# Optimization experiments

Hardware: AMD Instinct MI355X
Metric: run time of the kernel (lower is better)

Reference implementation:

```python
import jax, jax.numpy as jnp
import numpy as np

N_HEADS = 16


def setup_inputs() -> dict:
    key = jax.random.key(0)
    ks = jax.random.split(key, 9)
    B, S, D = 2, 2048, 1024
    s = 0.02
    return {
        "x": jax.random.normal(ks[0], (B, S, D), dtype=jnp.float32),
        "Wq": jax.random.normal(ks[1], (D, D), dtype=jnp.float32) * s,
        "bq": jax.random.normal(ks[2], (D,), dtype=jnp.float32) * s,
        "Wk": jax.random.normal(ks[3], (D, D), dtype=jnp.float32) * s,
        "bk": jax.random.normal(ks[4], (D,), dtype=jnp.float32) * s,
        "Wv": jax.random.normal(ks[5], (D, D), dtype=jnp.float32) * s,
        "bv": jax.random.normal(ks[6], (D,), dtype=jnp.float32) * s,
        "Wo": jax.random.normal(ks[7], (D, D), dtype=jnp.float32) * s,
        "bo": jax.random.normal(ks[8], (D,), dtype=jnp.float32) * s,
    }


def reference(x, Wq, bq, Wk, bk, Wv, bv, Wo, bo):
    B, S, D = x.shape
    H = N_HEADS
    hd = D // H
    # projections -> [B, H, S, hd]
    def heads(w, b):
        return (x @ w + b).reshape(B, S, H, hd).transpose(0, 2, 1, 3)
    Q, K, V = heads(Wq, bq), heads(Wk, bk), heads(Wv, bv)
    scores = jnp.einsum("bhqd,bhkd->bhqk", Q, K)
    causal = jnp.triu(jnp.ones((S, S), dtype=bool), k=1)  # True above diagonal
    scores = jnp.where(causal, -jnp.inf, scores)
    w = jax.nn.softmax(scores / jnp.sqrt(jnp.float32(hd)), axis=-1)
    ctx = jnp.einsum("bhqk,bhkd->bhqd", w, V).transpose(0, 2, 1, 3).reshape(B, S, D)
    return ctx @ Wo + bo
```

## Files before the change

### kernel.cpp

```cpp
#include <hip/hip_runtime.h>
#include <hip/hip_bf16.h>

typedef __attribute__((ext_vector_type(8))) short short8;
typedef __attribute__((ext_vector_type(4))) float floatx4;
typedef __attribute__((ext_vector_type(4))) int intx4;

#define D_MODEL 1024
#define SEQ     2048
#define NB      2
#define NH      16
#define HD      64
#define MROWS   4096
#define CZ      (0.125f * 1.44269504f)

__device__ __forceinline__ floatx4 mfma_bf16(short8 a, short8 b, floatx4 c) {
  return __builtin_amdgcn_mfma_f32_16x16x32_bf16(a, b, c, 0, 0, 0);
}

__device__ __forceinline__ void dma16(const __hip_bfloat16* g, __hip_bfloat16* l) {
  __builtin_amdgcn_global_load_lds(
      (const __attribute__((address_space(1))) void*)g,
      (__attribute__((address_space(3))) void*)l, 16, 0, 0);
}
#define WAIT_VM(n)  __asm__ __volatile__("s_waitcnt vmcnt(" #n ")" ::: "memory")
#define BARRIER()   __asm__ __volatile__("s_barrier" ::: "memory")
#define WAIT_LGKM() __asm__ __volatile__("s_waitcnt lgkmcnt(0)" ::: "memory")

__device__ __forceinline__ int pack2bf(float a, float b) {
  unsigned ua = __builtin_bit_cast(unsigned, a) + 0x8000u;
  unsigned ub = __builtin_bit_cast(unsigned, b) + 0x8000u;
  return (int)__builtin_amdgcn_perm(ub, ua, 0x07060302u);
}

__global__ void prep_kernel(const float* __restrict__ x, __hip_bfloat16* __restrict__ xb,
                            const float* __restrict__ W0, const float* __restrict__ W1,
                            const float* __restrict__ W2, const float* __restrict__ W3,
                            __hip_bfloat16* __restrict__ T0, __hip_bfloat16* __restrict__ T1,
                            __hip_bfloat16* __restrict__ T2, __hip_bfloat16* __restrict__ T3) {
  const int z = blockIdx.z;
  if (z == 4) {
    const int tid = threadIdx.y * 32 + threadIdx.x;
    const int base = ((blockIdx.y * 32 + blockIdx.x) * 256 + tid) * 16;
#pragma unroll
    for (int c = 0; c < 4; c++) {
      float4 v = *(const float4*)(x + base + c * 4);
      __hip_bfloat16 tmp[4];
      tmp[0] = __float2bfloat16(v.x);
      tmp[1] = __float2bfloat16(v.y);
      tmp[2] = __float2bfloat16(v.z);
      tmp[3] = __float2bfloat16(v.w);
      *(ushort4*)(xb + base + c * 4) = *(ushort4*)tmp;
    }
    return;
  }
  const float* W = (z == 0) ? W0 : (z == 1) ? W1 : (z == 2) ? W2 : W3;
  __hip_bfloat16* Wt = (z == 0) ? T0 : (z == 1) ? T1 : (z == 2) ? T2 : T3;
  __shared__ float tile[32][33];
  int k0 = blockIdx.x * 32, n0 = blockIdx.y * 32;
  int tx = threadIdx.x, ty = threadIdx.y;
#pragma unroll
  for (int i = 0; i < 4; i++)
    tile[ty + 8 * i][tx] = W[(size_t)(k0 + ty + 8 * i) * D_MODEL + n0 + tx];
  __syncthreads();
#pragma unroll
  for (int i = 0; i < 4; i++)
    Wt[(size_t)(n0 + ty + 8 * i) * D_MODEL + k0 + tx] = __float2bfloat16(tile[tx][ty + 8 * i]);
}

template <int MODE>
__global__ __launch_bounds__(256) void gemm_kernel(
    const __hip_bfloat16* __restrict__ X,
    const __hip_bfloat16* __restrict__ Wt0, const __hip_bfloat16* __restrict__ Wt1,
    const __hip_bfloat16* __restrict__ Wt2,
    const float* __restrict__ b0, const float* __restrict__ b1, const float* __restrict__ b2,
    void* __restrict__ out0, void* __restrict__ out1, void* __restrict__ out2) {
  constexpr int MT = (MODE == 0) ? 128 : 64;
  constexpr int I = MT / 32;
  constexpr int NKT = D_MODEL / 32;

  const int z = blockIdx.y;
  const __hip_bfloat16* Wt = (z == 0) ? Wt0 : (z == 1) ? Wt1 : Wt2;
  const float* bias = (z == 0) ? b0 : (z == 1) ? b1 : b2;
  void* outp = (z == 0) ? out0 : (z == 1) ? out1 : out2;
  const float scale = (MODE == 0 && z == 0) ? CZ : 1.f;

  __shared__ __attribute__((aligned(16))) __hip_bfloat16 As[3][MT * 32];
  __shared__ __attribute__((aligned(16))) __hip_bfloat16 Bs[3][128 * 32];

  const int n0 = blockIdx.x * 128;
  const int m0 = blockIdx.z * MT;
  const int t = threadIdx.x;
  const int lane = t & 63, w = t >> 6;
  const int wm = (w >> 1) * (MT / 2), wn = (w & 1) * 64;
  const int lr = lane & 15;
  const int lq = lane >> 4;

  const __hip_bfloat16* Xp = X + (size_t)m0 * D_MODEL;
  const __hip_bfloat16* Wp = Wt + (size_t)n0 * D_MODEL;

  const int lrow = lane >> 2;
  const int skg = (lane & 3) << 3;
  const int srowA = ((MT == 128) ? (w << 5) : (w << 4)) + lrow;
  const int sbA0 = (((MT == 128) ? (w << 5) : (w << 4)) << 5);
  const int sbA1 = sbA0 + (16 << 5);
  const int srowB = (w << 5) + lrow;
  const int sbB0 = ((w << 5) << 5);
  const int sbB1 = sbB0 + (16 << 5);

#define STAGE_G(kt_, buf_)                                                              \
  {                                                                                     \
    const int kn_ = (kt_) * 32;                                                         \
    dma16(Xp + (size_t)srowA * D_MODEL + kn_ + skg, &As[buf_][sbA0]);                   \
    if (MT == 128) dma16(Xp + (size_t)(srowA + 16) * D_MODEL + kn_ + skg, &As[buf_][sbA1]); \
    dma16(Wp + (size_t)srowB * D_MODEL + kn_ + skg, &Bs[buf_][sbB0]);                   \
    dma16(Wp + (size_t)(srowB + 16) * D_MODEL + kn_ + skg, &Bs[buf_][sbB1]);            \
  }

  floatx4 acc[I][4];
#pragma unroll
  for (int i = 0; i < I; i++)
#pragma unroll
    for (int j = 0; j < 4; j++) acc[i][j] = (floatx4){0.f, 0.f, 0.f, 0.f};

  STAGE_G(0, 0);
  STAGE_G(1, 1);

  int cb = 0;
  for (int kt = 0; kt < NKT; kt++) {
    if (kt < NKT - 1) {
      if constexpr (MODE == 0) WAIT_VM(4);
      else                     WAIT_VM(3);
    } else {
      WAIT_VM(0);
    }
    BARRIER();
    if (kt + 2 < NKT) {
      const int nb = (cb == 0) ? 2 : cb - 1;
      STAGE_G(kt + 2, nb);
    }
    const __hip_bfloat16* Ac = As[cb];
    const __hip_bfloat16* Bc = Bs[cb];
    short8 af[I], bfr[4];
#pragma unroll
    for (int i = 0; i < I; i++) af[i] = *(const short8*)&Ac[(wm + i * 16 + lr) * 32 + lq * 8];
#pragma unroll
    for (int j = 0; j < 4; j++) bfr[j] = *(const short8*)&Bc[(wn + j * 16 + lr) * 32 + lq * 8];
#pragma unroll
    for (int i = 0; i < I; i++)
#pragma unroll
      for (int j = 0; j < 4; j++) acc[i][j] = mfma_bf16(af[i], bfr[j], acc[i][j]);
    cb = (cb == 2) ? 0 : cb + 1;
  }
#undef STAGE_G

#pragma unroll
  for (int j = 0; j < 4; j++) {
    const int n = n0 + wn + j * 16 + lr;
    const float bv = bias[n];
#pragma unroll
    for (int i = 0; i < I; i++) {
      const int mb = m0 + wm + i * 16 + lq * 4;
      if (MODE == 0) {
        __hip_bfloat16* O = (__hip_bfloat16*)outp;
        const int b = mb >> 11, s = mb & 2047;
        const int h = n >> 6, d = n & 63;
        if (z == 2) {
          ushort4 pk;
          __hip_bfloat16* pp = (__hip_bfloat16*)&pk;
#pragma unroll
          for (int r = 0; r < 4; r++) pp[r] = __float2bfloat16(acc[i][j][r] + bv);
          *(ushort4*)(O + (((size_t)(b * NH + h) * HD + d) * SEQ + s)) = pk;
        } else {
#pragma unroll
          for (int r = 0; r < 4; r++)
            O[(((size_t)(b * NH + h) * SEQ + (s + r)) * HD) + d] =
                __float2bfloat16((acc[i][j][r] + bv) * scale);
        }
      } else {
#pragma unroll
        for (int r = 0; r < 4; r++)
          ((float*)outp)[(size_t)(mb + r) * D_MODEL + n] = acc[i][j][r] + bv;
      }
    }
  }
}

__global__ __launch_bounds__(256, 2) void attn_kernel(
    const __hip_bfloat16* __restrict__ Q, const __hip_bfloat16* __restrict__ Kg,
    const __hip_bfloat16* __restrict__ Vt, __hip_bfloat16* __restrict__ ctx) {
  const int bh = blockIdx.x;
  const int b = bh >> 4, h = bh & 15;
  const int p = blockIdx.y;
  const int t = threadIdx.x, lane = t & 63, w = t >> 6;
  const int lr = lane & 15, lq = lane >> 4;
  const int wr = w & 1, wb = w >> 1;

  __shared__ __attribute__((aligned(16))) __hip_bfloat16 Ks[2][128 * 64];
  __shared__ __attribute__((aligned(16))) __hip_bfloat16 VTs[2][64 * 128];
  __shared__ __attribute__((aligned(16))) float dumpO[2048];
  __shared__ float dumpL[256];

  const __hip_bfloat16* Qb = Q + (size_t)bh * SEQ * HD;
  const __hip_bfloat16* Kb = Kg + (size_t)bh * SEQ * HD;
  const __hip_bfloat16* Vb = Vt + (size_t)bh * HD * SEQ;

  short8 qf[2][2][2];
#pragma unroll
  for (int ph = 0; ph < 2; ph++) {
    const int qt = ph ? 31 - p : p;
#pragma unroll
    for (int rt = 0; rt < 2; rt++)
#pragma unroll
      for (int ks = 0; ks < 2; ks++)
        qf[ph][rt][ks] = *(const short8*)(Qb + (size_t)(qt * 64 + wr * 32 + rt * 16 + lr) * HD +
                                          ks * 32 + lq * 8);
  }

  const int krow = (w << 5) + (lane >> 3);
  const int ksl = lane & 7;
  const int vrow = (w << 4) + (lane >> 4);
  const int vsl = lane & 15;

#define STAGE(tb, nb)                                                                     \
  {                                                                                       \
    _Pragma("unroll") for (int i = 0; i < 4; i++) {                                       \
      const int r_ = krow + i * 8;                                                        \
      dma16(Kb + ((size_t)((tb) + r_) << 6) + ((ksl ^ (r_ & 7)) << 3),                    \
            &Ks[nb][((w << 5) + i * 8) << 6]);                                            \
    }                                                                                     \
    _Pragma("unroll") for (int i = 0; i < 4; i++) {                                       \
      const int r_ = vrow + i * 4;                                                        \
      dma16(Vb + (size_t)r_ * SEQ + (tb) + ((vsl ^ (r_ & 15)) << 3),                      \
            &VTs[nb][((w << 4) + i * 4) << 7]);                                           \
    }                                                                                     \
  }

  const int nktA = (p + 2) >> 1;
  const int TOT = 17;
#define KTN(gs) (((gs) < nktA) ? (gs) : (gs)-nktA)

  STAGE(0, 0);
  int g = 0;

  const int idx0 = (lr + ((lq & 1) << 5)) << 2;
  const int idx1 = idx0 + 64;
  const bool hi = (lq >= 2);

  const int kfb0 = (lr << 6) + ((lq ^ (lr & 7)) << 3);
  const int kfb1 = (lr << 6) + (((4 + lq) ^ (lr & 7)) << 3);
  const int vfb0 = (lr << 7) + ((((wb << 3) + lq) ^ lr) << 3);
  const int vfb1 = (lr << 7) + ((((wb << 3) + 4 + lq) ^ lr) << 3);
  const int kwoff = wb << 12;

  for (int ph = 0; ph < 2; ph++) {
    const int qt = ph ? 31 - p : p;
    const int nkt = (qt + 2) >> 1;
    const int qbase = qt * 64 + wr * 32;
    const int qmaxw = qbase + 31;

    floatx4 o[2][4];
#pragma unroll
    for (int rt = 0; rt < 2; rt++)
#pragma unroll
      for (int dt = 0; dt < 4; dt++) o[rt][dt] = (floatx4){0.f, 0.f, 0.f, 0.f};
    float ls[2] = {0.f, 0.f};

    for (int kt = 0; kt < nkt; kt++, g++) {
      WAIT_VM(0);
      BARRIER();
      if (g + 1 < TOT) STAGE(KTN(g + 1) << 7, (g + 1) & 1);

      const int n0w = (kt << 7) + (wb << 6);
      if (n0w <= qmaxw) {
        const int cbuf = g & 1;
        const __hip_bfloat16* Kc = &Ks[cbuf][kwoff];
        const __hip_bfloat16* Vc = VTs[cbuf];

        short8 kf[2][4];
#pragma unroll
        for (int nt = 0; nt < 4; nt++) {
          kf[0][nt] = *(const short8*)&Kc[(nt << 10) + kfb0];
          kf[1][nt] = *(const short8*)&Kc[(nt << 10) + kfb1];
        }
        floatx4 s[2][4];
#pragma unroll
        for (int rt = 0; rt < 2; rt++)
#pragma unroll
          for (int nt = 0; nt < 4; nt++) s[rt][nt] = (floatx4){0.f, 0.f, 0.f, 0.f};
#pragma unroll
        for (int ks = 0; ks < 2; ks++)
#pragma unroll
          for (int nt = 0; nt < 4; nt++) {
            s[0][nt] = mfma_bf16(kf[ks][nt], qf[ph][0][ks], s[0][nt]);
            s[1][nt] = mfma_bf16(kf[ks][nt], qf[ph][1][ks], s[1][nt]);
          }

        int pkA[2][4], pkB[2][4];
        const bool need_mask = (n0w + 63 > qbase);
#pragma unroll
        for (int rt = 0; rt < 2; rt++) {
          const int q = qbase + rt * 16 + lr;
#pragma unroll
          for (int nt = 0; nt < 4; nt++) {
            const int kbase = n0w + (nt << 4) + (lq << 2);
            float x0 = s[rt][nt][0], x1 = s[rt][nt][1], x2 = s[rt][nt][2], x3 = s[rt][nt][3];
            if (need_mask) {
              x0 = (kbase + 0 <= q) ? x0 : -1e30f;
              x1 = (kbase + 1 <= q) ? x1 : -1e30f;
              x2 = (kbase + 2 <= q) ? x2 : -1e30f;
              x3 = (kbase + 3 <= q) ? x3 : -1e30f;
            }
            const float p0 = __builtin_amdgcn_exp2f(x0);
            const float p1 = __builtin_amdgcn_exp2f(x1);
            const float p2 = __builtin_amdgcn_exp2f(x2);
            const float p3 = __builtin_amdgcn_exp2f(x3);
            ls[rt] += (p0 + p1) + (p2 + p3);
            pkA[rt][nt] = pack2bf(p0, p1);
            pkB[rt][nt] = pack2bf(p2, p3);
          }
        }

#pragma unroll
        for (int ks = 0; ks < 2; ks++) {
          short8 pf[2];
#pragma unroll
          for (int rt = 0; rt < 2; rt++) {
            const int t0 = 2 * ks, t1 = 2 * ks + 1;
            int c0a = __builtin_amdgcn_ds_bpermute(idx0, pkA[rt][t0]);
            int c0b = __builtin_amdgcn_ds_bpermute(idx0, pkA[rt][t1]);
            int c1a = __builtin_amdgcn_ds_bpermute(idx0, pkB[rt][t0]);
            int c1b = __builtin_amdgcn_ds_bpermute(idx0, pkB[rt][t1]);
            int c2a = __builtin_amdgcn_ds_bpermute(idx1, pkA[rt][t0]);
            int c2b = __builtin_amdgcn_ds_bpermute(idx1, pkA[rt][t1]);
            int c3a = __builtin_amdgcn_ds_bpermute(idx1, pkB[rt][t0]);
            int c3b = __builtin_amdgcn_ds_bpermute(idx1, pkB[rt][t1]);
            intx4 bi;
            bi[0] = hi ? c0b : c0a;
            bi[1] = hi ? c1b : c1a;
            bi[2] = hi ? c2b : c2a;
            bi[3] = hi ? c3b : c3a;
            pf[rt] = __builtin_bit_cast(short8, bi);
          }
          const int vfb = ks ? vfb1 : vfb0;
#pragma unroll
          for (int dt = 0; dt < 4; dt++) {
            short8 vf = *(const short8*)&Vc[(dt << 11) + vfb];
            o[0][dt] = mfma_bf16(vf, pf[0], o[0][dt]);
            o[1][dt] = mfma_bf16(vf, pf[1], o[1][dt]);
          }
        }
      }
    }

    const int dbase = (wr << 10) + (lane << 4);
    BARRIER();
    if (wb == 1) {
#pragma unroll
      for (int dt = 0; dt < 4; dt++) *(floatx4*)&dumpO[dbase + (dt << 2)] = o[0][dt];
      dumpL[(wr << 7) + (lane << 1)] = ls[0];
      dumpL[(wr << 7) + (lane << 1) + 1] = ls[1];
      WAIT_LGKM();
    }
    BARRIER();
    if (wb == 0) {
#pragma unroll
      for (int dt = 0; dt < 4; dt++) o[0][dt] += *(const floatx4*)&dumpO[dbase + (dt << 2)];
      ls[0] += dumpL[(wr << 7) + (lane << 1)];
      ls[1] += dumpL[(wr << 7) + (lane << 1) + 1];
    }
    BARRIER();
    if (wb == 1) {
#pragma unroll
      for (int dt = 0; dt < 4; dt++) *(floatx4*)&dumpO[dbase + (dt << 2)] = o[1][dt];
      WAIT_LGKM();
    }
    BARRIER();
    if (wb == 0) {
#pragma unroll
      for (int dt = 0; dt < 4; dt++) o[1][dt] += *(const floatx4*)&dumpO[dbase + (dt << 2)];
      float inv[2];
#pragma unroll
      for (int rt = 0; rt < 2; rt++) {
        float v = ls[rt];
        v += __shfl_xor(v, 16);
        v += __shfl_xor(v, 32);
        inv[rt] = 1.f / v;
      }
#pragma unroll
      for (int rt = 0; rt < 2; rt++) {
        const int row = qbase + rt * 16 + lr;
        __hip_bfloat16* cp = ctx + (size_t)b * SEQ * D_MODEL + (size_t)row * D_MODEL + h * HD;
#pragma unroll
        for (int dt = 0; dt < 4; dt++) {
          ushort4 pk;
          __hip_bfloat16* pp = (__hip_bfloat16*)&pk;
#pragma unroll
          for (int r = 0; r < 4; r++) pp[r] = __float2bfloat16(o[rt][dt][r] * inv[rt]);
          *(ushort4*)(cp + (dt << 4) + (lq << 2)) = pk;
        }
      }
    }
  }
#undef STAGE
#undef KTN
}

extern "C" void kernel_launch(void* const* d_in, const int* in_sizes, int n_in,
                              void* d_out, int out_size, void* d_ws, size_t ws_size,
                              hipStream_t stream) {
  const float* x  = (const float*)d_in[0];
  const float* Wq = (const float*)d_in[1];
  const float* bq = (const float*)d_in[2];
  const float* Wk = (const float*)d_in[3];
  const float* bk = (const float*)d_in[4];
  const float* Wv = (const float*)d_in[5];
  const float* bv = (const float*)d_in[6];
  const float* Wo = (const float*)d_in[7];
  const float* bo = (const float*)d_in[8];

  char* ws = (char*)d_ws;
  const size_t MB = 1u << 20;
  __hip_bfloat16* xb  = (__hip_bfloat16*)(ws + 0 * MB);
  __hip_bfloat16* wtq = (__hip_bfloat16*)(ws + 8 * MB);
  __hip_bfloat16* wtk = (__hip_bfloat16*)(ws + 10 * MB);
  __hip_bfloat16* wtv = (__hip_bfloat16*)(ws + 12 * MB);
  __hip_bfloat16* wto = (__hip_bfloat16*)(ws + 14 * MB);
  __hip_bfloat16* qb  = (__hip_bfloat16*)(ws + 16 * MB);
  __hip_bfloat16* kb  = (__hip_bfloat16*)(ws + 24 * MB);
  __hip_bfloat16* vt  = (__hip_bfloat16*)(ws + 32 * MB);
  __hip_bfloat16* ctx = xb;

  prep_kernel<<<dim3(32, 32, 5), dim3(32, 8), 0, stream>>>(x, xb, Wq, Wk, Wv, Wo,
                                                           wtq, wtk, wtv, wto);
  gemm_kernel<0><<<dim3(8, 3, 32), 256, 0, stream>>>(xb, wtq, wtk, wtv, bq, bk, bv,
                                                     (void*)qb, (void*)kb, (void*)vt);
  attn_kernel<<<dim3(32, 16), 256, 0, stream>>>(qb, kb, vt, ctx);
  gemm_kernel<1><<<dim3(8, 1, 64), 256, 0, stream>>>(ctx, wto, wto, wto, bo, bo, bo,
                                                     d_out, d_out, d_out);
}
```

Before: 194.6 us.

## Split attention into one block per query tile with 64-key tiles

Each attention block now handles one 64-row query tile instead of a pair of balanced tiles, and the grid doubles to 32x32, ordered heaviest-first. K/V tiles shrink from 128 to 64 keys, which halves shared memory so the reduction scratch can reuse the K/V buffers, and launch bounds rise to allow 4 blocks per CU. The aim is higher occupancy and more blocks to hide latency. The cost is more barriers per key, shorter per-iteration work, and reliance on heaviest-first scheduling for load balance.

```diff
diff --git a/kernel.cpp b/kernel.cpp
--- a/kernel.cpp
+++ b/kernel.cpp
@@ -185,224 +185,196 @@
   }
 }
 
-__global__ __launch_bounds__(256, 2) void attn_kernel(
+__global__ __launch_bounds__(256, 4) void attn_kernel(
     const __hip_bfloat16* __restrict__ Q, const __hip_bfloat16* __restrict__ Kg,
     const __hip_bfloat16* __restrict__ Vt, __hip_bfloat16* __restrict__ ctx) {
   const int bh = blockIdx.x;
   const int b = bh >> 4, h = bh & 15;
-  const int p = blockIdx.y;
+  const int qt = 31 - blockIdx.y;
   const int t = threadIdx.x, lane = t & 63, w = t >> 6;
   const int lr = lane & 15, lq = lane >> 4;
   const int wr = w & 1, wb = w >> 1;
 
-  __shared__ __attribute__((aligned(16))) __hip_bfloat16 Ks[2][128 * 64];
-  __shared__ __attribute__((aligned(16))) __hip_bfloat16 VTs[2][64 * 128];
-  __shared__ __attribute__((aligned(16))) float dumpO[2048];
-  __shared__ float dumpL[256];
+  __shared__ __attribute__((aligned(16))) __hip_bfloat16 Ks[2][64 * 64];
+  __shared__ __attribute__((aligned(16))) __hip_bfloat16 VTs[2][64 * 64];
 
   const __hip_bfloat16* Qb = Q + (size_t)bh * SEQ * HD;
   const __hip_bfloat16* Kb = Kg + (size_t)bh * SEQ * HD;
   const __hip_bfloat16* Vb = Vt + (size_t)bh * HD * SEQ;
 
-  short8 qf[2][2][2];
-#pragma unroll
-  for (int ph = 0; ph < 2; ph++) {
-    const int qt = ph ? 31 - p : p;
-#pragma unroll
-    for (int rt = 0; rt < 2; rt++)
-#pragma unroll
-      for (int ks = 0; ks < 2; ks++)
-        qf[ph][rt][ks] = *(const short8*)(Qb + (size_t)(qt * 64 + wr * 32 + rt * 16 + lr) * HD +
-                                          ks * 32 + lq * 8);
-  }
-
-  const int krow = (w << 5) + (lane >> 3);
-  const int ksl = lane & 7;
-  const int vrow = (w << 4) + (lane >> 4);
-  const int vsl = lane & 15;
-
-#define STAGE(tb, nb)                                                                     \
-  {                                                                                       \
-    _Pragma("unroll") for (int i = 0; i < 4; i++) {                                       \
-      const int r_ = krow + i * 8;                                                        \
-      dma16(Kb + ((size_t)((tb) + r_) << 6) + ((ksl ^ (r_ & 7)) << 3),                    \
-            &Ks[nb][((w << 5) + i * 8) << 6]);                                            \
-    }                                                                                     \
-    _Pragma("unroll") for (int i = 0; i < 4; i++) {                                       \
-      const int r_ = vrow + i * 4;                                                        \
-      dma16(Vb + (size_t)r_ * SEQ + (tb) + ((vsl ^ (r_ & 15)) << 3),                      \
-            &VTs[nb][((w << 4) + i * 4) << 7]);                                           \
-    }                                                                                     \
-  }
-
-  const int nktA = (p + 2) >> 1;
-  const int TOT = 17;
-#define KTN(gs) (((gs) < nktA) ? (gs) : (gs)-nktA)
-
+  const int qrow0 = qt * 64 + wr * 32;
+
+  short8 qf[2][2];
+#pragma unroll
+  for (int rt = 0; rt < 2; rt++)
+#pragma unroll
+    for (int ks = 0; ks < 2; ks++)
+      qf[rt][ks] = *(const short8*)(Qb + (size_t)(qrow0 + rt * 16 + lr) * HD + ks * 32 + lq * 8);
+
+  const int srow = (w << 4) + (lane >> 3);
+  const int sgl = lane & 7;
+  const int sb0 = (w << 4) << 6;
+  const int sb1 = ((w << 4) + 8) << 6;
+
+#define STAGE(tb, nb)                                                                  \
+  {                                                                                    \
+    const int r0 = srow, r1 = srow + 8;                                                \
+    dma16(Kb + ((size_t)((tb) + r0) << 6) + ((sgl ^ (r0 & 7)) << 3), &Ks[nb][sb0]);    \
+    dma16(Kb + ((size_t)((tb) + r1) << 6) + ((sgl ^ (r1 & 7)) << 3), &Ks[nb][sb1]);    \
+    dma16(Vb + (size_t)r0 * SEQ + (tb) + ((sgl ^ (r0 & 7)) << 3), &VTs[nb][sb0]);      \
+    dma16(Vb + (size_t)r1 * SEQ + (tb) + ((sgl ^ (r1 & 7)) << 3), &VTs[nb][sb1]);      \
+  }
+
+  const int nkt = qt + 1;
   STAGE(0, 0);
-  int g = 0;
+
+  floatx4 o[2][4];
+#pragma unroll
+  for (int rt = 0; rt < 2; rt++)
+#pragma unroll
+    for (int dt = 0; dt < 4; dt++) o[rt][dt] = (floatx4){0.f, 0.f, 0.f, 0.f};
+  float ls[2] = {0.f, 0.f};
 
   const int idx0 = (lr + ((lq & 1) << 5)) << 2;
   const int idx1 = idx0 + 64;
   const bool hi = (lq >= 2);
 
-  const int kfb0 = (lr << 6) + ((lq ^ (lr & 7)) << 3);
-  const int kfb1 = (lr << 6) + (((4 + lq) ^ (lr & 7)) << 3);
-  const int vfb0 = (lr << 7) + ((((wb << 3) + lq) ^ lr) << 3);
-  const int vfb1 = (lr << 7) + ((((wb << 3) + 4 + lq) ^ lr) << 3);
-  const int kwoff = wb << 12;
-
-  for (int ph = 0; ph < 2; ph++) {
-    const int qt = ph ? 31 - p : p;
-    const int nkt = (qt + 2) >> 1;
-    const int qbase = qt * 64 + wr * 32;
-    const int qmaxw = qbase + 31;
-
-    floatx4 o[2][4];
-#pragma unroll
-    for (int rt = 0; rt < 2; rt++)
-#pragma unroll
-      for (int dt = 0; dt < 4; dt++) o[rt][dt] = (floatx4){0.f, 0.f, 0.f, 0.f};
-    float ls[2] = {0.f, 0.f};
-
-    for (int kt = 0; kt < nkt; kt++, g++) {
-      WAIT_VM(0);
-      BARRIER();
-      if (g + 1 < TOT) STAGE(KTN(g + 1) << 7, (g + 1) & 1);
-
-      const int n0w = (kt << 7) + (wb << 6);
-      if (n0w <= qmaxw) {
-        const int cbuf = g & 1;
-        const __hip_bfloat16* Kc = &Ks[cbuf][kwoff];
-        const __hip_bfloat16* Vc = VTs[cbuf];
-
-        short8 kf[2][4];
-#pragma unroll
-        for (int nt = 0; nt < 4; nt++) {
-          kf[0][nt] = *(const short8*)&Kc[(nt << 10) + kfb0];
-          kf[1][nt] = *(const short8*)&Kc[(nt << 10) + kfb1];
+  const int kfb0 = ((wb << 4) + lr) << 6;
+  const int kg0 = ((lq ^ (lr & 7)) << 3);
+  const int kg1 = (((4 + lq) ^ (lr & 7)) << 3);
+  const int vg = ((((lq & 2) << 1) + (wb << 1) + (lq & 1)) ^ (lr & 7)) << 3;
+
+  for (int kt = 0; kt < nkt; kt++) {
+    WAIT_VM(0);
+    BARRIER();
+    if (kt + 1 < nkt) STAGE((kt + 1) << 6, (kt + 1) & 1);
+
+    const int kw0 = (kt << 6) + (wb << 4);
+    if (kw0 <= qrow0 + 31) {
+      const __hip_bfloat16* Kc = Ks[kt & 1];
+      const __hip_bfloat16* Vc = VTs[kt & 1];
+
+      short8 kf[2][2];
+#pragma unroll
+      for (int nt = 0; nt < 2; nt++) {
+        kf[0][nt] = *(const short8*)&Kc[(nt << 11) + kfb0 + kg0];
+        kf[1][nt] = *(const short8*)&Kc[(nt << 11) + kfb0 + kg1];
+      }
+      floatx4 s[2][2];
+#pragma unroll
+      for (int rt = 0; rt < 2; rt++)
+#pragma unroll
+        for (int nt = 0; nt < 2; nt++) s[rt][nt] = (floatx4){0.f, 0.f, 0.f, 0.f};
+#pragma unroll
+      for (int ks = 0; ks < 2; ks++)
+#pragma unroll
+        for (int nt = 0; nt < 2; nt++) {
+          s[0][nt] = mfma_bf16(kf[ks][nt], qf[0][ks], s[0][nt]);
+          s[1][nt] = mfma_bf16(kf[ks][nt], qf[1][ks], s[1][nt]);
         }
-        floatx4 s[2][4];
-#pragma unroll
-        for (int rt = 0; rt < 2; rt++)
-#pragma unroll
-          for (int nt = 0; nt < 4; nt++) s[rt][nt] = (floatx4){0.f, 0.f, 0.f, 0.f};
-#pragma unroll
-        for (int ks = 0; ks < 2; ks++)
-#pragma unroll
-          for (int nt = 0; nt < 4; nt++) {
-            s[0][nt] = mfma_bf16(kf[ks][nt], qf[ph][0][ks], s[0][nt]);
-            s[1][nt] = mfma_bf16(kf[ks][nt], qf[ph][1][ks], s[1][nt]);
+
+      const bool need_mask = (kw0 + 47 > qrow0);
+      int pkA[2][2], pkB[2][2];
+#pragma unroll
+      for (int rt = 0; rt < 2; rt++) {
+        const int q = qrow0 + rt * 16 + lr;
+#pragma unroll
+        for (int nt = 0; nt < 2; nt++) {
+          const int kbase = (kt << 6) + (nt << 5) + (wb << 4) + (lq << 2);
+          float x0 = s[rt][nt][0], x1 = s[rt][nt][1], x2 = s[rt][nt][2], x3 = s[rt][nt][3];
+          if (need_mask) {
+            x0 = (kbase + 0 <= q) ? x0 : -1e30f;
+            x1 = (kbase + 1 <= q) ? x1 : -1e30f;
+            x2 = (kbase + 2 <= q) ? x2 : -1e30f;
+            x3 = (kbase + 3 <= q) ? x3 : -1e30f;
           }
-
-        int pkA[2][4], pkB[2][4];
-        const bool need_mask = (n0w + 63 > qbase);
-#pragma unroll
-        for (int rt = 0; rt < 2; rt++) {
-          const int q = qbase + rt * 16 + lr;
-#pragma unroll
-          for (int nt = 0; nt < 4; nt++) {
-            const int kbase = n0w + (nt << 4) + (lq << 2);
-            float x0 = s[rt][nt][0], x1 = s[rt][nt][1], x2 = s[rt][nt][2], x3 = s[rt][nt][3];
-            if (need_mask) {
-              x0 = (kbase + 0 <= q) ? x0 : -1e30f;
-              x1 = (kbase + 1 <= q) ? x1 : -1e30f;
-              x2 = (kbase + 2 <= q) ? x2 : -1e30f;
-              x3 = (kbase + 3 <= q) ? x3 : -1e30f;
-            }
-            const float p0 = __builtin_amdgcn_exp2f(x0);
-            const float p1 = __builtin_amdgcn_exp2f(x1);
-            const float p2 = __builtin_amdgcn_exp2f(x2);
-            const float p3 = __builtin_amdgcn_exp2f(x3);
-            ls[rt] += (p0 + p1) + (p2 + p3);
-            pkA[rt][nt] = pack2bf(p0, p1);
-            pkB[rt][nt] = pack2bf(p2, p3);
-          }
+          const float p0 = __builtin_amdgcn_exp2f(x0);
+          const float p1 = __builtin_amdgcn_exp2f(x1);
+          const float p2 = __builtin_amdgcn_exp2f(x2);
+          const float p3 = __builtin_amdgcn_exp2f(x3);
+          ls[rt] += (p0 + p1) + (p2 + p3);
+          pkA[rt][nt] = pack2bf(p0, p1);
+          pkB[rt][nt] = pack2bf(p2, p3);
         }
-
-#pragma unroll
-        for (int ks = 0; ks < 2; ks++) {
-          short8 pf[2];
-#pragma unroll
-          for (int rt = 0; rt < 2; rt++) {
-            const int t0 = 2 * ks, t1 = 2 * ks + 1;
-            int c0a = __builtin_amdgcn_ds_bpermute(idx0, pkA[rt][t0]);
-            int c0b = __builtin_amdgcn_ds_bpermute(idx0, pkA[rt][t1]);
-            int c1a = __builtin_amdgcn_ds_bpermute(idx0, pkB[rt][t0]);
-            int c1b = __builtin_amdgcn_ds_bpermute(idx0, pkB[rt][t1]);
-            int c2a = __builtin_amdgcn_ds_bpermute(idx1, pkA[rt][t0]);
-            int c2b = __builtin_amdgcn_ds_bpermute(idx1, pkA[rt][t1]);
-            int c3a = __builtin_amdgcn_ds_bpermute(idx1, pkB[rt][t0]);
-            int c3b = __builtin_amdgcn_ds_bpermute(idx1, pkB[rt][t1]);
-            intx4 bi;
-            bi[0] = hi ? c0b : c0a;
-            bi[1] = hi ? c1b : c1a;
-            bi[2] = hi ? c2b : c2a;
-            bi[3] = hi ? c3b : c3a;
-            pf[rt] = __builtin_bit_cast(short8, bi);
-          }
-          const int vfb = ks ? vfb1 : vfb0;
-#pragma unroll
-          for (int dt = 0; dt < 4; dt++) {
-            short8 vf = *(const short8*)&Vc[(dt << 11) + vfb];
-            o[0][dt] = mfma_bf16(vf, pf[0], o[0][dt]);
-            o[1][dt] = mfma_bf16(vf, pf[1], o[1][dt]);
-          }
-        }
-      }
-    }
-
-    const int dbase = (wr << 10) + (lane << 4);
-    BARRIER();
-    if (wb == 1) {
-#pragma unroll
-      for (int dt = 0; dt < 4; dt++) *(floatx4*)&dumpO[dbase + (dt << 2)] = o[0][dt];
-      dumpL[(wr << 7) + (lane << 1)] = ls[0];
-      dumpL[(wr << 7) + (lane << 1) + 1] = ls[1];
-      WAIT_LGKM();
-    }
-    BARRIER();
-    if (wb == 0) {
-#pragma unroll
-      for (int dt = 0; dt < 4; dt++) o[0][dt] += *(const floatx4*)&dumpO[dbase + (dt << 2)];
-      ls[0] += dumpL[(wr << 7) + (lane << 1)];
-      ls[1] += dumpL[(wr << 7) + (lane << 1) + 1];
-    }
-    BARRIER();
-    if (wb == 1) {
-#pragma unroll
-      for (int dt = 0; dt < 4; dt++) *(floatx4*)&dumpO[dbase + (dt << 2)] = o[1][dt];
-      WAIT_LGKM();
-    }
-    BARRIER();
-    if (wb == 0) {
-#pragma unroll
-      for (int dt = 0; dt < 4; dt++) o[1][dt] += *(const floatx4*)&dumpO[dbase + (dt << 2)];
-      float inv[2];
+      }
+
+      short8 pf[2];
 #pragma unroll
       for (int rt = 0; rt < 2; rt++) {
-        float v = ls[rt];
-        v += __shfl_xor(v, 16);
-        v += __shfl_xor(v, 32);
-        inv[rt] = 1.f / v;
-      }
-#pragma unroll
-      for (int rt = 0; rt < 2; rt++) {
-        const int row = qbase + rt * 16 + lr;
-        __hip_bfloat16* cp = ctx + (size_t)b * SEQ * D_MODEL + (size_t)row * D_MODEL + h * HD;
-#pragma unroll
-        for (int dt = 0; dt < 4; dt++) {
-          ushort4 pk;
-          __hip_bfloat16* pp = (__hip_bfloat16*)&pk;
-#pragma unroll
-          for (int r = 0; r < 4; r++) pp[r] = __float2bfloat16(o[rt][dt][r] * inv[rt]);
-          *(ushort4*)(cp + (dt << 4) + (lq << 2)) = pk;
-        }
+        int c0a = __builtin_amdgcn_ds_bpermute(idx0, pkA[rt][0]);
+        int c0b = __builtin_amdgcn_ds_bpermute(idx0, pkA[rt][1]);
+        int c1a = __builtin_amdgcn_ds_bpermute(idx0, pkB[rt][0]);
+        int c1b = __builtin_amdgcn_ds_bpermute(idx0, pkB[rt][1]);
+        int c2a = __builtin_amdgcn_ds_bpermute(idx1, pkA[rt][0]);
+        int c2b = __builtin_amdgcn_ds_bpermute(idx1, pkA[rt][1]);
+        int c3a = __builtin_amdgcn_ds_bpermute(idx1, pkB[rt][0]);
+        int c3b = __builtin_amdgcn_ds_bpermute(idx1, pkB[rt][1]);
+        intx4 bi;
+        bi[0] = hi ? c0b : c0a;
+        bi[1] = hi ? c1b : c1a;
+        bi[2] = hi ? c2b : c2a;
+        bi[3] = hi ? c3b : c3a;
+        pf[rt] = __builtin_bit_cast(short8, bi);
+      }
+#pragma unroll
+      for (int dt = 0; dt < 4; dt++) {
+        short8 vf = *(const short8*)&Vc[(((dt << 4) + lr) << 6) + vg];
+        o[0][dt] = mfma_bf16(vf, pf[0], o[0][dt]);
+        o[1][dt] = mfma_bf16(vf, pf[1], o[1][dt]);
+      }
+    }
+  }
+
+  BARRIER();
+  if (wb == 1) {
+    float* d0 = (float*)&Ks[0][0];
+    float* d1 = (float*)&Ks[1][0];
+    float* dl = (float*)&VTs[0][0];
+    const int base = (wr << 10) + (lane << 4);
+#pragma unroll
+    for (int dt = 0; dt < 4; dt++) *(floatx4*)&d0[base + (dt << 2)] = o[0][dt];
+#pragma unroll
+    for (int dt = 0; dt < 4; dt++) *(floatx4*)&d1[base + (dt << 2)] = o[1][dt];
+    dl[(wr << 7) + (lane << 1)] = ls[0];
+    dl[(wr << 7) + (lane << 1) + 1] = ls[1];
+    WAIT_LGKM();
+  }
+  BARRIER();
+  if (wb == 0) {
+    const float* d0 = (const float*)&Ks[0][0];
+    const float* d1 = (const float*)&Ks[1][0];
+    const float* dl = (const float*)&VTs[0][0];
+    const int base = (wr << 10) + (lane << 4);
+#pragma unroll
+    for (int dt = 0; dt < 4; dt++) {
+      o[0][dt] += *(const floatx4*)&d0[base + (dt << 2)];
+      o[1][dt] += *(const floatx4*)&d1[base + (dt << 2)];
+    }
+    ls[0] += dl[(wr << 7) + (lane << 1)];
+    ls[1] += dl[(wr << 7) + (lane << 1) + 1];
+    float inv[2];
+#pragma unroll
+    for (int rt = 0; rt < 2; rt++) {
+      float v = ls[rt];
+      v += __shfl_xor(v, 16);
+      v += __shfl_xor(v, 32);
+      inv[rt] = 1.f / v;
+    }
+#pragma unroll
+    for (int rt = 0; rt < 2; rt++) {
+      const int row = qrow0 + rt * 16 + lr;
+      __hip_bfloat16* cp = ctx + (size_t)b * SEQ * D_MODEL + (size_t)row * D_MODEL + h * HD;
+#pragma unroll
+      for (int dt = 0; dt < 4; dt++) {
+        ushort4 pk;
+        __hip_bfloat16* pp = (__hip_bfloat16*)&pk;
+#pragma unroll
+        for (int r = 0; r < 4; r++) pp[r] = __float2bfloat16(o[rt][dt][r] * inv[rt]);
+        *(ushort4*)(cp + (dt << 4) + (lq << 2)) = pk;
       }
     }
   }
 #undef STAGE
-#undef KTN
 }
 
 extern "C" void kernel_launch(void* const* d_in, const int* in_sizes, int n_in,
@@ -434,7 +406,7 @@
                                                            wtq, wtk, wtv, wto);
   gemm_kernel<0><<<dim3(8, 3, 32), 256, 0, stream>>>(xb, wtq, wtk, wtv, bq, bk, bv,
                                                      (void*)qb, (void*)kb, (void*)vt);
-  attn_kernel<<<dim3(32, 16), 256, 0, stream>>>(qb, kb, vt, ctx);
+  attn_kernel<<<dim3(32, 32), 256, 0, stream>>>(qb, kb, vt, ctx);
   gemm_kernel<1><<<dim3(8, 1, 64), 256, 0, stream>>>(ctx, wto, wto, wto, bo, bo, bo,
                                                      d_out, d_out, d_out);
 }
```

Result: no change. 192.3 us (-1.2%).
